# Performance work log

Measured on AMD Instinct MI355X. Metric: run time of the kernel, lower is better.

## Reference

```python
import jax, jax.numpy as jnp
from jax import lax
import numpy as np

B, P, M1, M2, M3 = 128, 168, 2, 2, 2
M = M1 * M2 * M3
HIDC, HIDR, HIDS, CK, SKIP, HW = 50, 50, 5, 6, 24, 24
PT = (P - CK) // SKIP  # int((P-Ck)/skip) = 6
L = P - CK + 1         # 163


def gru(xs, w_ih, w_hh, b_ih, b_hh, hid):
    # xs: [T, N, in]; torch nn.GRU cell semantics, h0 = 0. Returns final h: [N, hid].
    def step(h, x):
        gi = x @ w_ih.T + b_ih
        gh = h @ w_hh.T + b_hh
        ir, iz, inn = jnp.split(gi, 3, axis=-1)
        hr, hz, hn = jnp.split(gh, 3, axis=-1)
        r = jax.nn.sigmoid(ir + hr)
        z = jax.nn.sigmoid(iz + hz)
        n = jnp.tanh(inn + r * hn)
        return (1.0 - z) * n + z * h, None
    h0 = jnp.zeros((xs.shape[1], hid), xs.dtype)
    h, _ = lax.scan(step, h0, xs)
    return h


def setup_inputs() -> dict:
    key = jax.random.key(0)
    ks = jax.random.split(key, 16)
    O = P * HIDC * CK  # 50400 conv output channels
    d = {
        'x': jax.random.normal(ks[0], (B, P, M1, M2, M3), jnp.float32),
        'conv_w': jax.random.normal(ks[1], (O, P, M1, M2, M3), jnp.float32) * 0.02,
        'conv_b': jax.random.normal(ks[2], (O,), jnp.float32) * 0.02,
        'g1_wih': jax.random.normal(ks[3], (3 * HIDR, HIDC), jnp.float32) * 0.1,
        'g1_whh': jax.random.normal(ks[4], (3 * HIDR, HIDR), jnp.float32) * 0.1,
        'g1_bih': jax.random.normal(ks[5], (3 * HIDR,), jnp.float32) * 0.1,
        'g1_bhh': jax.random.normal(ks[6], (3 * HIDR,), jnp.float32) * 0.1,
        'gs_wih': jax.random.normal(ks[7], (3 * HIDS, HIDC), jnp.float32) * 0.1,
        'gs_whh': jax.random.normal(ks[8], (3 * HIDS, HIDS), jnp.float32) * 0.1,
        'gs_bih': jax.random.normal(ks[9], (3 * HIDS,), jnp.float32) * 0.1,
        'gs_bhh': jax.random.normal(ks[10], (3 * HIDS,), jnp.float32) * 0.1,
        'l1_w': jax.random.normal(ks[11], (M, HIDR + SKIP * HIDS), jnp.float32) * 0.1,
        'l1_b': jax.random.normal(ks[12], (M,), jnp.float32) * 0.1,
        'hw_w': jax.random.normal(ks[13], (1, HW), jnp.float32) * 0.1,
        'hw_b': jax.random.normal(ks[14], (1,), jnp.float32) * 0.1,
    }
    return d


def reference(x, conv_w, conv_b, g1_wih, g1_whh, g1_bih, g1_bhh,
              gs_wih, gs_whh, gs_bih, gs_bhh, l1_w, l1_b, hw_w, hw_b):
    # Conv3d with kernel == full spatial extent is a dense matmul over (P*m1*m2*m3).
    xf = x.reshape(B, -1)                       # [B, P*M]
    wf = conv_w.reshape(conv_w.shape[0], -1)    # [O, P*M]
    c = jax.nn.relu(xf @ wf.T + conv_b)         # [B, O]
    c = c.reshape(B, HIDC, CK, P)
    # Diagonal strided sum (the torch triple loop): res1[b,c,t] = sum_k c[b,c,k,k+t]
    res1 = sum(c[:, :, k, k:k + L] for k in range(CK))  # [B, HIDC, L]
    # dropout: eval mode (identity)
    r = gru(jnp.transpose(res1, (2, 0, 1)), g1_wih, g1_whh, g1_bih, g1_bhh, HIDR)  # [B, HIDR]
    # skip GRU
    s = res1[:, :, -PT * SKIP:]                          # [B, HIDC, PT*SKIP]
    s = s.reshape(B, HIDC, PT, SKIP)
    s = jnp.transpose(s, (2, 0, 3, 1)).reshape(PT, B * SKIP, HIDC)
    hs = gru(s, gs_wih, gs_whh, gs_bih, gs_bhh, HIDS)    # [B*SKIP, HIDS]
    hs = hs.reshape(B, SKIP * HIDS)
    r = jnp.concatenate([r, hs], axis=1)                 # [B, HIDR + SKIP*HIDS]
    res = r @ l1_w.T + l1_b                              # [B, M]
    # highway (AR) component over the last HW timesteps
    z = x[:, -HW:].reshape(B, HW, M)                     # [B, HW, M]
    z = jnp.transpose(z, (0, 2, 1)).reshape(-1, HW)      # [B*M, HW]
    z = z @ hw_w.T + hw_b                                # [B*M, 1]
    res = res + z.reshape(B, M)
    res = jax.nn.sigmoid(res)
    return res.reshape(B, M1, M2, M3)
```

## Files before the change

kernel.cpp:

```cpp
#include <hip/hip_runtime.h>
#include <hip/hip_bf16.h>
#include <cstdint>


typedef __attribute__((ext_vector_type(8))) short short8;
typedef __attribute__((ext_vector_type(4))) float f32x4;
typedef __attribute__((ext_vector_type(2))) float f32x2;

__device__ __forceinline__ unsigned short bf16rn(float f) {
    unsigned u = __float_as_uint(f);
    return (unsigned short)((u + 0x7FFFu + ((u >> 16) & 1u)) >> 16);
}
__device__ __forceinline__ unsigned pk2(float a, float b) {
    return ((unsigned)bf16rn(b) << 16) | (unsigned)bf16rn(a);
}
__device__ __forceinline__ uint4 pack8(float4 f0, float4 f1) {
    uint4 u;
    u.x = pk2(f0.x, f0.y); u.y = pk2(f0.z, f0.w);
    u.z = pk2(f1.x, f1.y); u.w = pk2(f1.z, f1.w);
    return u;
}
__device__ __forceinline__ float bf2f(unsigned short u) {
    return __uint_as_float((unsigned)u << 16);
}
__device__ __forceinline__ float sigmf(float x) {
    return __builtin_amdgcn_rcpf(1.f + __expf(-x));
}
__device__ __forceinline__ float tanhf_(float x) {
    return 1.f - 2.f * __builtin_amdgcn_rcpf(__expf(2.f * x) + 1.f);
}

__global__ __launch_bounds__(256, 2)
void k1_conv_gemm(const float* __restrict__ x, const float* __restrict__ w,
                  const float* __restrict__ bias, unsigned short* __restrict__ c) {
    __shared__ uint4 a_lds[8 * 129];
    __shared__ uint4 b_lds[8 * 113];
    const int tid  = threadIdx.x;
    const int n0   = blockIdx.x * 112;
    const int wave = tid >> 6, lane = tid & 63;
    const int quad = lane >> 4, m16 = lane & 15;

    f32x4 acc[2][7];
#pragma unroll
    for (int i = 0; i < 2; ++i)
#pragma unroll
        for (int j = 0; j < 7; ++j) acc[i][j] = (f32x4){0.f, 0.f, 0.f, 0.f};

    float4 pa[4][2];
    float4 pb[4][2];

    auto issue = [&](int kb) {
#pragma unroll
        for (int i = 0; i < 4; ++i) {
            int row = (tid >> 3) + 32 * i;
            const float* gp = x + row * 1344 + kb + (tid & 7) * 8;
            pa[i][0] = *reinterpret_cast<const float4*>(gp);
            pa[i][1] = *reinterpret_cast<const float4*>(gp + 4);
        }
#pragma unroll
        for (int i = 0; i < 4; ++i) {
            int idx = tid + 256 * i;
            if (idx < 896) {
                int row = idx >> 3;
                const float* gp = w + (size_t)(n0 + row) * 1344 + kb + (idx & 7) * 8;
                pb[i][0] = *reinterpret_cast<const float4*>(gp);
                pb[i][1] = *reinterpret_cast<const float4*>(gp + 4);
            }
        }
    };

    issue(0);
    for (int kb = 0; kb < 1344; kb += 64) {
#pragma unroll
        for (int i = 0; i < 4; ++i) {
            int idx = tid + 256 * i;
            int row = idx >> 3, ks = idx & 7;
            a_lds[ks * 129 + row] = pack8(pa[i][0], pa[i][1]);
        }
#pragma unroll
        for (int i = 0; i < 4; ++i) {
            int idx = tid + 256 * i;
            if (idx < 896) {
                int row = idx >> 3, ks = idx & 7;
                b_lds[ks * 113 + row] = pack8(pb[i][0], pb[i][1]);
            }
        }
        __syncthreads();
        if (kb + 64 < 1344) issue(kb + 64);
#pragma unroll
        for (int half = 0; half < 2; ++half) {
            const int kp = half * 4 + quad;
            short8 af[2], bfr[7];
#pragma unroll
            for (int rt = 0; rt < 2; ++rt)
                af[rt] = ((const short8*)a_lds)[kp * 129 + wave * 32 + rt * 16 + m16];
#pragma unroll
            for (int ct = 0; ct < 7; ++ct)
                bfr[ct] = ((const short8*)b_lds)[kp * 113 + ct * 16 + m16];
#pragma unroll
            for (int rt = 0; rt < 2; ++rt)
#pragma unroll
                for (int ct = 0; ct < 7; ++ct)
                    acc[rt][ct] = __builtin_amdgcn_mfma_f32_16x16x32_bf16(
                        af[rt], bfr[ct], acc[rt][ct], 0, 0, 0);
        }
        __syncthreads();
    }
#pragma unroll
    for (int ct = 0; ct < 7; ++ct) {
        int col = n0 + ct * 16 + m16;
        float bv = bias[col];
#pragma unroll
        for (int rt = 0; rt < 2; ++rt) {
#pragma unroll
            for (int r = 0; r < 4; ++r) {
                int grow = wave * 32 + rt * 16 + quad * 4 + r;
                float v = acc[rt][ct][r] + bv;
                v = fmaxf(v, 0.f);
                c[(size_t)grow * 50400 + col] = bf16rn(v);
            }
        }
    }
}

__global__ __launch_bounds__(384, 1)
void k_proj(const unsigned short* __restrict__ c,
            const float* __restrict__ g1_wih, const float* __restrict__ g1_bih,
            const float* __restrict__ gs_wih, const float* __restrict__ gs_bih,
            float* __restrict__ gi1g, float* __restrict__ gi2g) {
    __shared__ float rloc[50 * 164];
    __shared__ __align__(8) float gi1l[163 * 150];
    __shared__ __align__(8) float gi2l[144 * 15];

    const int b    = blockIdx.x;
    const int tid  = threadIdx.x;
    const int wave = tid >> 6, lane = tid & 63;

    const unsigned short* cb = c + (size_t)b * 50400;
    for (int idx = tid; idx < 8150; idx += 384) {
        int hc = idx / 163, t = idx - hc * 163;
        int base = hc * 1008 + t;
        float s = 0.f;
#pragma unroll
        for (int k = 0; k < 6; ++k) s += bf2f(cb[base + 169 * k]);
        rloc[hc * 164 + t] = s;
    }
    __syncthreads();

    {
        const int tB   = (wave >> 1) * 64 + lane;
        const int half = wave & 1;
        if (tB < 163) {
            float xcol[50];
#pragma unroll
            for (int j = 0; j < 50; ++j) xcol[j] = rloc[j * 164 + tB];

            const int c0 = __builtin_amdgcn_readfirstlane(half * 75);
            const float* wbase = g1_wih + c0 * 50;
            float* gdst = &gi1l[tB * 150 + c0];
            for (int cc = 0; cc < 75; ++cc) {
                const float* wp = wbase + cc * 50;
                float acc = g1_bih[c0 + cc];
#pragma unroll
                for (int j = 0; j < 50; ++j) acc += xcol[j] * wp[j];
                gdst[cc] = acc;
            }
            if (tB >= 19) {
                const int r2 = tB - 19;
                const int d0 = __builtin_amdgcn_readfirstlane(half * 8);
                const int ncol = half ? 7 : 8;
                float* g2 = &gi2l[r2 * 15];
                for (int cc = 0; cc < ncol; ++cc) {
                    const float* wp = gs_wih + (d0 + cc) * 50;
                    float acc = gs_bih[d0 + cc];
#pragma unroll
                    for (int j = 0; j < 50; ++j) acc += xcol[j] * wp[j];
                    g2[d0 + cc] = acc;
                }
            }
        }
    }
    __syncthreads();

    {
        const float2* src = reinterpret_cast<const float2*>(gi1l);
        float2* dst = reinterpret_cast<float2*>(gi1g + (size_t)b * 24450);
        for (int i = tid; i < 12225; i += 384) dst[i] = src[i];
        const float2* s2 = reinterpret_cast<const float2*>(gi2l);
        float2* d2 = reinterpret_cast<float2*>(gi2g + (size_t)b * 2160);
        for (int i = tid; i < 1080; i += 384) d2[i] = s2[i];
    }
}

__global__ __launch_bounds__(64, 1)
void k_gru(const float* __restrict__ gi1g, const float* __restrict__ g1_whh,
           const float* __restrict__ g1_bhh,
           const float* __restrict__ gi2g, const float* __restrict__ gs_whh,
           const float* __restrict__ gs_bhh,
           const float* __restrict__ l1_w, const float* __restrict__ l1_b,
           const float* __restrict__ x, const float* __restrict__ hw_w,
           const float* __restrict__ hw_b, float* __restrict__ out) {
    __shared__ __align__(16) float hl[64];
    __shared__ float r1l[50];
    __shared__ float hsl[120];

    const int b = blockIdx.x;
    const int lane = threadIdx.x;
    const int lc = (lane < 50) ? lane : 49;

    f32x2 wr2[25], wz2[25], wn2[25];
    {
        const float* wrp = g1_whh + lc * 50;
        const float* wzp = g1_whh + (50 + lc) * 50;
        const float* wnp = g1_whh + (100 + lc) * 50;
#pragma unroll
        for (int j = 0; j < 25; ++j) {
            wr2[j] = *reinterpret_cast<const f32x2*>(wrp + 2 * j);
            wz2[j] = *reinterpret_cast<const f32x2*>(wzp + 2 * j);
            wn2[j] = *reinterpret_cast<const f32x2*>(wnp + 2 * j);
        }
#pragma unroll
        for (int j = 0; j < 25; ++j) {
            asm volatile("" : "+v"(wr2[j]));
            asm volatile("" : "+v"(wz2[j]));
            asm volatile("" : "+v"(wn2[j]));
        }
    }
    const float bhr = g1_bhh[lc], bhz = g1_bhh[50 + lc], bhn = g1_bhh[100 + lc];
    hl[lane] = 0.f;
    float hcur = 0.f;

    const float* gp = gi1g + (size_t)b * 24450;
    float gir = gp[lc], giz = gp[50 + lc], gin = gp[100 + lc];
    for (int t = 0; t < 163; ++t) {
        float ngir = 0.f, ngiz = 0.f, ngin = 0.f;
        if (t < 162) {
            const float* gq = gp + 150;
            ngir = gq[lc]; ngiz = gq[50 + lc]; ngin = gq[100 + lc];
        }
        float4 h4[12];
#pragma unroll
        for (int j4 = 0; j4 < 12; ++j4)
            h4[j4] = *reinterpret_cast<const float4*>(&hl[4 * j4]);
        f32x2 ht; ht.x = hl[48]; ht.y = hl[49];
        f32x2 ar = {0.f, 0.f}, az = {0.f, 0.f}, an = {0.f, 0.f};
#pragma unroll
        for (int j4 = 0; j4 < 12; ++j4) {
            f32x2 h0; h0.x = h4[j4].x; h0.y = h4[j4].y;
            f32x2 h1; h1.x = h4[j4].z; h1.y = h4[j4].w;
            ar += wr2[2 * j4] * h0; ar += wr2[2 * j4 + 1] * h1;
            az += wz2[2 * j4] * h0; az += wz2[2 * j4 + 1] * h1;
            an += wn2[2 * j4] * h0; an += wn2[2 * j4 + 1] * h1;
        }
        ar += wr2[24] * ht; az += wz2[24] * ht; an += wn2[24] * ht;
        float rg = sigmf(gir + bhr + ar.x + ar.y);
        float zg = sigmf(giz + bhz + az.x + az.y);
        float ng = tanhf_(gin + rg * (bhn + an.x + an.y));
        hcur = (1.f - zg) * ng + zg * hcur;
        hl[lane] = hcur;
        gir = ngir; giz = ngiz; gin = ngin;
        gp += 150;
    }
    if (lane < 50) r1l[lane] = hcur;

    if (lane < 24) {
        float h2[5] = {0.f, 0.f, 0.f, 0.f, 0.f};
        const float* g2base = gi2g + (size_t)b * 2160;
        for (int pt = 0; pt < 6; ++pt) {
            const float* g2 = g2base + (pt * 24 + lane) * 15;
            float gi[15];
#pragma unroll
            for (int i = 0; i < 15; ++i) gi[i] = g2[i];
            float gh[15];
#pragma unroll
            for (int i = 0; i < 15; ++i) {
                float s = gs_bhh[i];
#pragma unroll
                for (int j = 0; j < 5; ++j) s += gs_whh[i * 5 + j] * h2[j];
                gh[i] = s;
            }
#pragma unroll
            for (int u = 0; u < 5; ++u) {
                float rg = sigmf(gi[u] + gh[u]);
                float zg = sigmf(gi[5 + u] + gh[5 + u]);
                float ng = tanhf_(gi[10 + u] + rg * gh[10 + u]);
                h2[u] = (1.f - zg) * ng + zg * h2[u];
            }
        }
#pragma unroll
        for (int u = 0; u < 5; ++u) hsl[lane * 5 + u] = h2[u];
    }

    if (lane < 8) {
        const int m = lane;
        float acc = l1_b[m];
        const float* wrow = l1_w + m * 170;
#pragma unroll
        for (int j = 0; j < 50; ++j) acc += r1l[j] * wrow[j];
#pragma unroll
        for (int j = 0; j < 120; ++j) acc += hsl[j] * wrow[50 + j];
        float z = hw_b[0];
        const float* xb = x + (size_t)b * 1344 + 144 * 8 + m;
#pragma unroll
        for (int wi = 0; wi < 24; ++wi) z += xb[wi * 8] * hw_w[wi];
        out[b * 8 + m] = __builtin_amdgcn_rcpf(1.f + __expf(-(acc + z)));
    }
}

extern "C" void kernel_launch(void* const* d_in, const int* in_sizes, int n_in,
                              void* d_out, int out_size, void* d_ws, size_t ws_size,
                              hipStream_t stream) {
    const float* x      = (const float*)d_in[0];
    const float* conv_w = (const float*)d_in[1];
    const float* conv_b = (const float*)d_in[2];
    const float* g1_wih = (const float*)d_in[3];
    const float* g1_whh = (const float*)d_in[4];
    const float* g1_bih = (const float*)d_in[5];
    const float* g1_bhh = (const float*)d_in[6];
    const float* gs_wih = (const float*)d_in[7];
    const float* gs_whh = (const float*)d_in[8];
    const float* gs_bih = (const float*)d_in[9];
    const float* gs_bhh = (const float*)d_in[10];
    const float* l1_w   = (const float*)d_in[11];
    const float* l1_b   = (const float*)d_in[12];
    const float* hw_w   = (const float*)d_in[13];
    const float* hw_b   = (const float*)d_in[14];
    float* out = (float*)d_out;

    char* ws = (char*)d_ws;
    unsigned short* c = (unsigned short*)ws;
    float* gi1g       = (float*)(ws + 12902400);
    float* gi2g       = (float*)(ws + 25420800);

    hipLaunchKernelGGL(k1_conv_gemm, dim3(450), dim3(256), 0, stream, x, conv_w, conv_b, c);
    hipLaunchKernelGGL(k_proj,       dim3(128), dim3(384), 0, stream,
                       c, g1_wih, g1_bih, gs_wih, gs_bih, gi1g, gi2g);
    hipLaunchKernelGGL(k_gru,        dim3(128), dim3(64),  0, stream,
                       gi1g, g1_whh, g1_bhh, gi2g, gs_whh, gs_bhh,
                       l1_w, l1_b, x, hw_w, hw_b, out);
}
```

Measured before the change: 516.7 us.

## Fuse diagonal strided sum into conv GEMM epilogue via float atomics

The conv GEMM epilogue no longer writes the full bf16 intermediate of 128x50400 values. It now atomically adds each ReLU'd value into a compact fp32 res1 buffer of 128x50x163, which a new zero-init kernel clears first. k_proj then reads res1 directly instead of doing the 6-way diagonal sum, cutting intermediate memory traffic. In exchange it adds atomic contention (6-way per address), an extra launch, and non-deterministic fp32 summation order; the GRU loop also folds hidden biases into the preloaded inputs and uses an fma for the update.

```diff
diff --git a/kernel.cpp b/kernel.cpp
--- a/kernel.cpp
+++ b/kernel.cpp
@@ -20,9 +20,6 @@
     u.z = pk2(f1.x, f1.y); u.w = pk2(f1.z, f1.w);
     return u;
 }
-__device__ __forceinline__ float bf2f(unsigned short u) {
-    return __uint_as_float((unsigned)u << 16);
-}
 __device__ __forceinline__ float sigmf(float x) {
     return __builtin_amdgcn_rcpf(1.f + __expf(-x));
 }
@@ -30,9 +27,15 @@
     return 1.f - 2.f * __builtin_amdgcn_rcpf(__expf(2.f * x) + 1.f);
 }
 
+__global__ __launch_bounds__(256)
+void k0_zero(float* __restrict__ p) {
+    int i = blockIdx.x * 256 + threadIdx.x;
+    if (i < 260800) reinterpret_cast<float4*>(p)[i] = (float4){0.f, 0.f, 0.f, 0.f};
+}
+
 __global__ __launch_bounds__(256, 2)
 void k1_conv_gemm(const float* __restrict__ x, const float* __restrict__ w,
-                  const float* __restrict__ bias, unsigned short* __restrict__ c) {
+                  const float* __restrict__ bias, float* __restrict__ res1) {
     __shared__ uint4 a_lds[8 * 129];
     __shared__ uint4 b_lds[8 * 113];
     const int tid  = threadIdx.x;
@@ -110,21 +113,27 @@
     for (int ct = 0; ct < 7; ++ct) {
         int col = n0 + ct * 16 + m16;
         float bv = bias[col];
+        unsigned uc = (unsigned)col;
+        unsigned hc = uc / 1008u;
+        unsigned q  = uc - hc * 1008u;
+        unsigned kk = q / 169u;
+        unsigned t  = q - kk * 169u;
+        bool valid = (t < 163u);
+        float* dst = res1 + hc * 163u + t;
 #pragma unroll
         for (int rt = 0; rt < 2; ++rt) {
 #pragma unroll
             for (int r = 0; r < 4; ++r) {
                 int grow = wave * 32 + rt * 16 + quad * 4 + r;
-                float v = acc[rt][ct][r] + bv;
-                v = fmaxf(v, 0.f);
-                c[(size_t)grow * 50400 + col] = bf16rn(v);
+                float v = fmaxf(acc[rt][ct][r] + bv, 0.f);
+                if (valid) atomicAdd(dst + (size_t)grow * 8150u, v);
             }
         }
     }
 }
 
 __global__ __launch_bounds__(384, 1)
-void k_proj(const unsigned short* __restrict__ c,
+void k_proj(const float* __restrict__ res1g,
             const float* __restrict__ g1_wih, const float* __restrict__ g1_bih,
             const float* __restrict__ gs_wih, const float* __restrict__ gs_bih,
             float* __restrict__ gi1g, float* __restrict__ gi2g) {
@@ -136,14 +145,12 @@
     const int tid  = threadIdx.x;
     const int wave = tid >> 6, lane = tid & 63;
 
-    const unsigned short* cb = c + (size_t)b * 50400;
-    for (int idx = tid; idx < 8150; idx += 384) {
-        int hc = idx / 163, t = idx - hc * 163;
-        int base = hc * 1008 + t;
-        float s = 0.f;
-#pragma unroll
-        for (int k = 0; k < 6; ++k) s += bf2f(cb[base + 169 * k]);
-        rloc[hc * 164 + t] = s;
+    {
+        const float* src = res1g + (size_t)b * 8150;
+        for (int idx = tid; idx < 8150; idx += 384) {
+            int hc = idx / 163, t = idx - hc * 163;
+            rloc[hc * 164 + t] = src[idx];
+        }
     }
     __syncthreads();
 
@@ -231,12 +238,12 @@
     float hcur = 0.f;
 
     const float* gp = gi1g + (size_t)b * 24450;
-    float gir = gp[lc], giz = gp[50 + lc], gin = gp[100 + lc];
+    float gir = gp[lc] + bhr, giz = gp[50 + lc] + bhz, gin = gp[100 + lc];
     for (int t = 0; t < 163; ++t) {
         float ngir = 0.f, ngiz = 0.f, ngin = 0.f;
         if (t < 162) {
             const float* gq = gp + 150;
-            ngir = gq[lc]; ngiz = gq[50 + lc]; ngin = gq[100 + lc];
+            ngir = gq[lc] + bhr; ngiz = gq[50 + lc] + bhz; ngin = gq[100 + lc];
         }
         float4 h4[12];
 #pragma unroll
@@ -253,10 +260,10 @@
             an += wn2[2 * j4] * h0; an += wn2[2 * j4 + 1] * h1;
         }
         ar += wr2[24] * ht; az += wz2[24] * ht; an += wn2[24] * ht;
-        float rg = sigmf(gir + bhr + ar.x + ar.y);
-        float zg = sigmf(giz + bhz + az.x + az.y);
+        float rg = sigmf(gir + ar.x + ar.y);
+        float zg = sigmf(giz + az.x + az.y);
         float ng = tanhf_(gin + rg * (bhn + an.x + an.y));
-        hcur = (1.f - zg) * ng + zg * hcur;
+        hcur = fmaf(zg, hcur - ng, ng);
         hl[lane] = hcur;
         gir = ngir; giz = ngiz; gin = ngin;
         gp += 150;
@@ -328,14 +335,15 @@
     float* out = (float*)d_out;
 
     char* ws = (char*)d_ws;
-    unsigned short* c = (unsigned short*)ws;
-    float* gi1g       = (float*)(ws + 12902400);
-    float* gi2g       = (float*)(ws + 25420800);
-
-    hipLaunchKernelGGL(k1_conv_gemm, dim3(450), dim3(256), 0, stream, x, conv_w, conv_b, c);
-    hipLaunchKernelGGL(k_proj,       dim3(128), dim3(384), 0, stream,
-                       c, g1_wih, g1_bih, gs_wih, gs_bih, gi1g, gi2g);
-    hipLaunchKernelGGL(k_gru,        dim3(128), dim3(64),  0, stream,
+    float* res1g = (float*)ws;
+    float* gi1g  = (float*)(ws + 4172800);
+    float* gi2g  = (float*)(ws + 16691200);
+
+    hipLaunchKernelGGL(k0_zero,      dim3(1019), dim3(256), 0, stream, res1g);
+    hipLaunchKernelGGL(k1_conv_gemm, dim3(450),  dim3(256), 0, stream, x, conv_w, conv_b, res1g);
+    hipLaunchKernelGGL(k_proj,       dim3(128),  dim3(384), 0, stream,
+                       res1g, g1_wih, g1_bih, gs_wih, gs_bih, gi1g, gi2g);
+    hipLaunchKernelGGL(k_gru,        dim3(128),  dim3(64),  0, stream,
                        gi1g, g1_whh, g1_bhh, gi2g, gs_whh, gs_bhh,
                        l1_w, l1_b, x, hw_w, hw_b, out);
 }
```

Result: slower. 551.6 us (+6.8%).
